# Optimization experiments

Measured on AMD Instinct MI355X. Metric: run time of the kernel, lower is better.

## Reference

```python
import jax, jax.numpy as jnp
import numpy as np

WORLD_SIZE = 1
EXPERT_NUM = 8
D_MODEL = 1024
D_HIDDEN = 4096
TOK_PER_EXPERT = 2048


def setup_inputs() -> dict:
    key = jax.random.key(0)
    k1, k2, k3 = jax.random.split(key, 3)
    x = jax.random.normal(k1, (EXPERT_NUM, TOK_PER_EXPERT, D_MODEL), dtype=jnp.float32)
    # kaiming_uniform-like scale for faithfulness of magnitudes
    bound1 = 1.0 / np.sqrt(D_MODEL)
    bound2 = 1.0 / np.sqrt(D_HIDDEN)
    weight1 = jax.random.uniform(k2, (EXPERT_NUM, D_HIDDEN, D_MODEL), dtype=jnp.float32, minval=-bound1, maxval=bound1)
    weight2 = jax.random.uniform(k3, (EXPERT_NUM, D_MODEL, D_HIDDEN), dtype=jnp.float32, minval=-bound2, maxval=bound2)
    return {"x": x, "weight1": weight1, "weight2": weight2}


def reference(x, weight1, weight2):
    # x -> (world_size, expert_num, tokens, d_model)
    xr = x.reshape(WORLD_SIZE, EXPERT_NUM, -1, D_MODEL)
    # grouped GEMM 1 + ReLU: [g,e,s,m] x [e,h,m] -> [g,e,s,h]
    ffn1 = jax.nn.relu(jnp.einsum('gesm,ehm->gesh', xr, weight1))
    # grouped GEMM 2: [g,e,s,h] x [e,m,h] -> [g,e,s,m]
    y = jnp.einsum('gesh,emh->gesm', ffn1, weight2)
    return y
```

## Files before the change

### kernel.cpp

```cpp
#include <hip/hip_runtime.h>
#include <hip/hip_bf16.h>

#define EXPERTS 8
#define TOK 2048
#define DM 1024
#define DH 4096

#define BM 128
#define BN 128
#define BK 32
#define LSTR 40

typedef __bf16 bf16x8 __attribute__((ext_vector_type(8)));
typedef float  f32x4  __attribute__((ext_vector_type(4)));

static __device__ __forceinline__ bf16x8 cvt8(float4 a, float4 b) {
    bf16x8 r;
    r[0] = (__bf16)a.x; r[1] = (__bf16)a.y; r[2] = (__bf16)a.z; r[3] = (__bf16)a.w;
    r[4] = (__bf16)b.x; r[5] = (__bf16)b.y; r[6] = (__bf16)b.z; r[7] = (__bf16)b.w;
    return r;
}

static __device__ __forceinline__ void gload16(const __bf16* g, __bf16* l) {
    __builtin_amdgcn_global_load_lds(
        (__attribute__((address_space(1))) void*)g,
        (__attribute__((address_space(3))) void*)l, 16, 0, 0);
}

#define BARRIER() asm volatile("s_barrier" ::: "memory")
#define LGKM0()   do { asm volatile("s_waitcnt lgkmcnt(0)" ::: "memory"); \
                       __builtin_amdgcn_sched_barrier(0); } while (0)
#define LGKM8()   asm volatile("s_waitcnt lgkmcnt(8)" ::: "memory")
#define VMW4()    asm volatile("s_waitcnt vmcnt(4)" ::: "memory")
#define VMW0()    asm volatile("s_waitcnt vmcnt(0)" ::: "memory")

__global__ __launch_bounds__(256)
void cvt_all(const float* __restrict__ x,  const float* __restrict__ w1,
             const float* __restrict__ w2, __bf16* __restrict__ xb,
             __bf16* __restrict__ w1b,     __bf16* __restrict__ w2b,
             int nx, int nw1, int ntot) {
    int i = blockIdx.x * blockDim.x + threadIdx.x;
    const int stride = gridDim.x * blockDim.x;
    for (; i < ntot; i += stride) {
        const float* src; __bf16* dst; int off;
        if (i < nx)            { src = x;  dst = xb;  off = i; }
        else if (i < nx + nw1) { src = w1; dst = w1b; off = i - nx; }
        else                   { src = w2; dst = w2b; off = i - nx - nw1; }
        const float4* p = (const float4*)src + (size_t)off * 2;
        float4 a = p[0], b = p[1];
        *((bf16x8*)dst + off) = cvt8(a, b);
    }
}

template<bool RELU, bool OUT_BF16>
__global__ __launch_bounds__(512, 2)
void gemm8(const __bf16* __restrict__ Ap, const __bf16* __restrict__ Bp,
           void* __restrict__ Cp, int N, int K, int tiles_m, int tiles_n,
           size_t sA, size_t sB, size_t sC)
{
    __shared__ __bf16 lds[2][2][16384];

    int bid = blockIdx.x;
    const int chunk = gridDim.x >> 3;
    bid = (bid & 7) * chunk + (bid >> 3);

    const int per_e = tiles_m * tiles_n;
    const int e  = bid / per_e;
    const int tt = bid - e * per_e;
    const int tn = tt / tiles_m;
    const int tm = tt - tn * tiles_m;

    const int tid = threadIdx.x;
    const int l   = tid & 63;
    const int wid = tid >> 6;
    const int wr  = wid >> 2;
    const int wc  = wid & 3;
    const int lr  = l & 15;
    const int kg  = l >> 4;
    const int lq  = l >> 3;
    const int swz_e = ((l & 7) ^ lq) << 3;

    const int cc0  = (kg * 16) ^ ((l & 7) << 4);
    const int cc1  = cc0 ^ 64;
    const int rowA = (wr * 128 + lr) * 128;
    const int rowB = (wc * 64  + lr) * 128;

    const __bf16* Ag = Ap + e * sA + (size_t)(tm * 256) * K;
    const __bf16* Bg = Bp + e * sB + (size_t)(tn * 256) * K;

    auto stage_half = [&](const __bf16* g, int mat, int c2, int h, int kt2) {
        const __bf16* s0 = g + (size_t)(h * 128 + wid * 8 + lq) * K + kt2 * 64 + swz_e;
        gload16(s0,                  &lds[c2][mat][h * 8192 + wid * 512]);
        gload16(s0 + (size_t)64 * K, &lds[c2][mat][h * 8192 + 4096 + wid * 512]);
    };

    f32x4 acc[8][4];
    #pragma unroll
    for (int m = 0; m < 8; ++m)
        #pragma unroll
        for (int n = 0; n < 4; ++n)
            acc[m][n] = (f32x4){0.f, 0.f, 0.f, 0.f};

    const char* A0b = (const char*)&lds[0][0][0] + rowA;
    const char* B0b = (const char*)&lds[0][1][0] + rowB;
    const char* A1b = (const char*)&lds[1][0][0] + rowA;
    const char* B1b = (const char*)&lds[1][1][0] + rowB;

    bf16x8 al[4][2], ah[4][2], bl[2][2], bh[2][2];

    auto rdA = [&](bf16x8 (&dst)[4][2], const char* base, int half) {
        #pragma unroll
        for (int mf = 0; mf < 4; ++mf) {
            dst[mf][0] = *(const bf16x8*)(base + (half * 4 + mf) * 2048 + cc0);
            dst[mf][1] = *(const bf16x8*)(base + (half * 4 + mf) * 2048 + cc1);
        }
    };
    auto rdB = [&](bf16x8 (&dst)[2][2], const char* base, int half) {
        #pragma unroll
        for (int nf = 0; nf < 2; ++nf) {
            dst[nf][0] = *(const bf16x8*)(base + (half * 2 + nf) * 2048 + cc0);
            dst[nf][1] = *(const bf16x8*)(base + (half * 2 + nf) * 2048 + cc1);
        }
    };
    auto mma16 = [&](bf16x8 (&af)[4][2], bf16x8 (&bf_)[2][2], int mo, int no) {
        __builtin_amdgcn_s_setprio(1);
        #pragma unroll
        for (int mf = 0; mf < 4; ++mf)
            #pragma unroll
            for (int nf = 0; nf < 2; ++nf) {
                acc[mo + mf][no + nf] = __builtin_amdgcn_mfma_f32_16x16x32_bf16(af[mf][0], bf_[nf][0], acc[mo + mf][no + nf], 0, 0, 0);
                acc[mo + mf][no + nf] = __builtin_amdgcn_mfma_f32_16x16x32_bf16(af[mf][1], bf_[nf][1], acc[mo + mf][no + nf], 0, 0, 0);
            }
        __builtin_amdgcn_s_setprio(0);
    };

    const int NT = K / 64;
    const int NI = NT / 2;

    stage_half(Ag, 0, 0, 0, 0); stage_half(Ag, 0, 0, 1, 0);
    stage_half(Bg, 1, 0, 0, 0); stage_half(Bg, 1, 0, 1, 0);
    stage_half(Bg, 1, 1, 0, 1); stage_half(Bg, 1, 1, 1, 1);
    VMW4();
    BARRIER();

    for (int it = 0; it < NI; ++it) {
        const int To = 2 * it + 1;
        const int Te = 2 * it + 2;
        const int Tn = 2 * it + 3;
        const bool pf = (it + 1 < NI);

        rdA(al, A0b, 0); rdB(bl, B0b, 0);
        stage_half(Ag, 0, 1, 0, To);
        LGKM8();
        BARRIER(); LGKM0();
        mma16(al, bl, 0, 0);
        BARRIER();

        rdB(bh, B0b, 1);
        stage_half(Ag, 0, 1, 1, To);
        BARRIER(); LGKM0();
        mma16(al, bh, 0, 2);
        BARRIER();

        rdA(ah, A0b, 1);
        if (pf) stage_half(Bg, 1, 0, 0, Te);
        BARRIER(); LGKM0();
        mma16(ah, bh, 4, 2);
        BARRIER();

        if (pf) stage_half(Bg, 1, 0, 1, Te);
        BARRIER();
        mma16(ah, bl, 4, 0);
        if (pf) VMW4(); else VMW0();
        BARRIER();

        rdA(al, A1b, 0); rdB(bl, B1b, 0);
        if (pf) stage_half(Ag, 0, 0, 0, Te);
        LGKM8();
        BARRIER(); LGKM0();
        mma16(al, bl, 0, 0);
        BARRIER();

        rdB(bh, B1b, 1);
        if (pf) stage_half(Ag, 0, 0, 1, Te);
        BARRIER(); LGKM0();
        mma16(al, bh, 0, 2);
        BARRIER();

        rdA(ah, A1b, 1);
        if (pf) stage_half(Bg, 1, 1, 0, Tn);
        BARRIER(); LGKM0();
        mma16(ah, bh, 4, 2);
        BARRIER();

        if (pf) stage_half(Bg, 1, 1, 1, Tn);
        BARRIER();
        mma16(ah, bl, 4, 0);
        if (pf) VMW4();
        BARRIER();
    }

    const int orow = tm * 256 + wr * 128 + kg * 4;
    const int ocol = tn * 256 + wc * 64 + lr;
    if constexpr (OUT_BF16) {
        __bf16* C = (__bf16*)Cp + e * sC;
        #pragma unroll
        for (int mf = 0; mf < 8; ++mf)
            #pragma unroll
            for (int j = 0; j < 4; ++j) {
                const size_t base = (size_t)(orow + mf * 16 + j) * N + ocol;
                #pragma unroll
                for (int nf = 0; nf < 4; ++nf) {
                    float v = acc[mf][nf][j];
                    if (RELU) v = fmaxf(v, 0.f);
                    C[base + nf * 16] = (__bf16)v;
                }
            }
    } else {
        float* C = (float*)Cp + e * sC;
        #pragma unroll
        for (int mf = 0; mf < 8; ++mf)
            #pragma unroll
            for (int j = 0; j < 4; ++j) {
                const size_t base = (size_t)(orow + mf * 16 + j) * N + ocol;
                #pragma unroll
                for (int nf = 0; nf < 4; ++nf) {
                    float v = acc[mf][nf][j];
                    if (RELU) v = fmaxf(v, 0.f);
                    C[base + nf * 16] = v;
                }
            }
    }
}

template<int AMODE, int BMODE, bool RELU, bool OUT_BF16>
__global__ __launch_bounds__(256)
void gemm2(const void* __restrict__ Ap, const void* __restrict__ Bp,
           void* __restrict__ Cp, int N, int K, int tiles_m, int tiles_n,
           size_t sA, size_t sB, size_t sC)
{
    constexpr int LA = (AMODE == 0) ? BK : LSTR;
    constexpr int LB = (BMODE == 0) ? BK : LSTR;
    __shared__ __bf16 As[BM * LA];
    __shared__ __bf16 Bs[BN * LB];

    int bid = blockIdx.x;
    const int chunk = gridDim.x >> 3;
    bid = (bid & 7) * chunk + (bid >> 3);

    const int per_e = tiles_m * tiles_n;
    const int e  = bid / per_e;
    const int t  = bid - e * per_e;
    const int tn = t / tiles_m;
    const int tm = t - tn * tiles_m;

    const int tid = threadIdx.x;
    const int l   = tid & 63;
    const int wid = tid >> 6;
    const int wr  = wid >> 1, wc = wid & 1;
    const int lr  = l & 15;
    const int kg  = l >> 4;
    const int srow = tid >> 1;
    const int scol = (tid & 1) << 4;

    const __bf16* gA = nullptr; __bf16* lA = nullptr;
    const float*  pAf = nullptr; __bf16* aWr = nullptr;
    float4 A0, A1, A2, A3;
    if constexpr (AMODE == 0) {
        gA = (const __bf16*)Ap + e * sA
           + (size_t)(tm * BM + wid * 16 + (l >> 2)) * K + (l & 3) * 8;
        lA = As + wid * 512;
    } else {
        pAf = (const float*)Ap + e * sA + (size_t)(tm * BM + srow) * K + scol;
        aWr = As + srow * LA + scol;
        A0 = *(const float4*)(pAf);      A1 = *(const float4*)(pAf + 4);
        A2 = *(const float4*)(pAf + 8);  A3 = *(const float4*)(pAf + 12);
    }
    const __bf16* gB = nullptr; __bf16* lB = nullptr;
    const float*  pBf = nullptr; __bf16* bWr = nullptr;
    float4 B0, B1, B2, B3;
    if constexpr (BMODE == 0) {
        gB = (const __bf16*)Bp + e * sB
           + (size_t)(tn * BN + wid * 16 + (l >> 2)) * K + (l & 3) * 8;
        lB = Bs + wid * 512;
    } else {
        pBf = (const float*)Bp + e * sB + (size_t)(tn * BN + srow) * K + scol;
        bWr = Bs + srow * LB + scol;
        B0 = *(const float4*)(pBf);      B1 = *(const float4*)(pBf + 4);
        B2 = *(const float4*)(pBf + 8);  B3 = *(const float4*)(pBf + 12);
    }

    const __bf16* aRd = As + (wr * 64 + lr) * LA + kg * 8;
    const __bf16* bRd = Bs + (wc * 64 + lr) * LB + kg * 8;

    f32x4 acc[4][4];
    #pragma unroll
    for (int m = 0; m < 4; ++m)
        #pragma unroll
        for (int n = 0; n < 4; ++n)
            acc[m][n] = (f32x4){0.f, 0.f, 0.f, 0.f};

    const int NT = K / BK;
    for (int kt = 0; kt < NT; ++kt) {
        if (kt) __syncthreads();
        if constexpr (AMODE == 0) {
            gload16(gA, lA);
            gload16(gA + (size_t)64 * K, lA + 2048);
            gA += BK;
        } else {
            *(bf16x8*)(aWr)     = cvt8(A0, A1);
            *(bf16x8*)(aWr + 8) = cvt8(A2, A3);
        }
        if constexpr (BMODE == 0) {
            gload16(gB, lB);
            gload16(gB + (size_t)64 * K, lB + 2048);
            gB += BK;
        } else {
            *(bf16x8*)(bWr)     = cvt8(B0, B1);
            *(bf16x8*)(bWr + 8) = cvt8(B2, B3);
        }
        __syncthreads();

        if (kt + 1 < NT) {
            if constexpr (AMODE == 2) {
                pAf += BK;
                A0 = *(const float4*)(pAf);      A1 = *(const float4*)(pAf + 4);
                A2 = *(const float4*)(pAf + 8);  A3 = *(const float4*)(pAf + 12);
            }
            if constexpr (BMODE == 2) {
                pBf += BK;
                B0 = *(const float4*)(pBf);      B1 = *(const float4*)(pBf + 4);
                B2 = *(const float4*)(pBf + 8);  B3 = *(const float4*)(pBf + 12);
            }
        }

        bf16x8 af[4], bfr[4];
        #pragma unroll
        for (int m = 0; m < 4; ++m) af[m]  = *(const bf16x8*)(aRd + m * 16 * LA);
        #pragma unroll
        for (int n = 0; n < 4; ++n) bfr[n] = *(const bf16x8*)(bRd + n * 16 * LB);
        #pragma unroll
        for (int m = 0; m < 4; ++m)
            #pragma unroll
            for (int n = 0; n < 4; ++n)
                acc[m][n] = __builtin_amdgcn_mfma_f32_16x16x32_bf16(af[m], bfr[n], acc[m][n], 0, 0, 0);
    }

    const int orow = tm * BM + wr * 64 + kg * 4;
    const int ocol = tn * BN + wc * 64 + lr;
    if constexpr (OUT_BF16) {
        __bf16* C = (__bf16*)Cp + e * sC;
        #pragma unroll
        for (int m = 0; m < 4; ++m)
            #pragma unroll
            for (int j = 0; j < 4; ++j) {
                const size_t base = (size_t)(orow + m * 16 + j) * N + ocol;
                #pragma unroll
                for (int n = 0; n < 4; ++n) {
                    float v = acc[m][n][j];
                    if (RELU) v = fmaxf(v, 0.f);
                    C[base + n * 16] = (__bf16)v;
                }
            }
    } else {
        float* C = (float*)Cp + e * sC;
        #pragma unroll
        for (int m = 0; m < 4; ++m)
            #pragma unroll
            for (int j = 0; j < 4; ++j) {
                const size_t base = (size_t)(orow + m * 16 + j) * N + ocol;
                #pragma unroll
                for (int n = 0; n < 4; ++n) {
                    float v = acc[m][n][j];
                    if (RELU) v = fmaxf(v, 0.f);
                    C[base + n * 16] = v;
                }
            }
    }
}

extern "C" void kernel_launch(void* const* d_in, const int* in_sizes, int n_in,
                              void* d_out, int out_size, void* d_ws, size_t ws_size,
                              hipStream_t stream) {
    const float* x  = (const float*)d_in[0];
    const float* w1 = (const float*)d_in[1];
    const float* w2 = (const float*)d_in[2];
    float* out = (float*)d_out;

    const size_t SZ_F  = (size_t)EXPERTS * TOK * DH * sizeof(__bf16);
    const size_t SZ_X  = (size_t)EXPERTS * TOK * DM * sizeof(__bf16);
    const size_t SZ_W1 = (size_t)EXPERTS * DH * DM * sizeof(__bf16);
    const size_t SZ_W2 = (size_t)EXPERTS * DM * DH * sizeof(__bf16);

    char* wsb = (char*)d_ws;
    __bf16* ffn1 = (__bf16*)wsb;

    const dim3 blk(256);
    const dim3 cgrid(2048);
    const int NX  = EXPERTS * TOK * DM / 8;
    const int NW1 = EXPERTS * DH * DM / 8;
    const int NW2 = EXPERTS * DM * DH / 8;

    const size_t eA1 = (size_t)TOK * DM, eB1 = (size_t)DH * DM, eC1 = (size_t)TOK * DH;
    const size_t eA2 = (size_t)TOK * DH, eB2 = (size_t)DM * DH, eC2 = (size_t)TOK * DM;

    if (ws_size >= SZ_F + SZ_X + SZ_W1 + SZ_W2) {
        __bf16* xb  = (__bf16*)(wsb + SZ_F);
        __bf16* w1b = (__bf16*)(wsb + SZ_F + SZ_X);
        __bf16* w2b = (__bf16*)(wsb + SZ_F + SZ_X + SZ_W1);
        hipLaunchKernelGGL(cvt_all, cgrid, blk, 0, stream,
            x, w1, w2, xb, w1b, w2b, NX, NW1, NX + NW1 + NW2);
        const dim3 g1(EXPERTS * (TOK / 256) * (DH / 256));
        const dim3 g2(EXPERTS * (TOK / 256) * (DM / 256));
        hipLaunchKernelGGL((gemm8<true, true>), g1, dim3(512), 0, stream,
            xb, w1b, ffn1, DH, DM, TOK / 256, DH / 256, eA1, eB1, eC1);
        hipLaunchKernelGGL((gemm8<false, false>), g2, dim3(512), 0, stream,
            ffn1, w2b, out, DM, DH, TOK / 256, DM / 256, eA2, eB2, eC2);
    } else if (ws_size >= SZ_F + SZ_X + SZ_W1) {
        __bf16* xb  = (__bf16*)(wsb + SZ_F);
        __bf16* w1b = (__bf16*)(wsb + SZ_F + SZ_X);
        hipLaunchKernelGGL(cvt_all, cgrid, blk, 0, stream,
            x, w1, w1, xb, w1b, w1b, NX, NW1, NX + NW1);
        const dim3 g1(EXPERTS * (TOK / 256) * (DH / 256));
        const dim3 g2(EXPERTS * (TOK / BM) * (DM / BN));
        hipLaunchKernelGGL((gemm8<true, true>), g1, dim3(512), 0, stream,
            xb, w1b, ffn1, DH, DM, TOK / 256, DH / 256, eA1, eB1, eC1);
        hipLaunchKernelGGL((gemm2<0, 2, false, false>), g2, blk, 0, stream,
            ffn1, w2, out, DM, DH, TOK / BM, DM / BN, eA2, eB2, eC2);
    } else if (ws_size >= SZ_F + SZ_W1) {
        __bf16* w1b = (__bf16*)(wsb + SZ_F);
        hipLaunchKernelGGL(cvt_all, cgrid, blk, 0, stream,
            w1, w1, w1, w1b, w1b, w1b, NW1, 0, NW1);
        const dim3 g1(EXPERTS * (TOK / BM) * (DH / BN));
        const dim3 g2(EXPERTS * (TOK / BM) * (DM / BN));
        hipLaunchKernelGGL((gemm2<2, 0, true, true>), g1, blk, 0, stream,
            x, w1b, ffn1, DH, DM, TOK / BM, DH / BN, eA1, eB1, eC1);
        hipLaunchKernelGGL((gemm2<0, 2, false, false>), g2, blk, 0, stream,
            ffn1, w2, out, DM, DH, TOK / BM, DM / BN, eA2, eB2, eC2);
    } else if (ws_size >= SZ_F) {
        const dim3 g1(EXPERTS * (TOK / BM) * (DH / BN));
        const dim3 g2(EXPERTS * (TOK / BM) * (DM / BN));
        hipLaunchKernelGGL((gemm2<2, 2, true, true>), g1, blk, 0, stream,
            x, w1, ffn1, DH, DM, TOK / BM, DH / BN, eA1, eB1, eC1);
        hipLaunchKernelGGL((gemm2<0, 2, false, false>), g2, blk, 0, stream,
            ffn1, w2, out, DM, DH, TOK / BM, DM / BN, eA2, eB2, eC2);
    } else {
        int rows = (int)((ws_size / ((size_t)DH * sizeof(__bf16))) / BM) * BM;
        if (rows <= 0) rows = BM;
        if (rows > TOK) rows = TOK;
        for (int e = 0; e < EXPERTS; ++e) {
            for (int r0 = 0; r0 < TOK; r0 += rows) {
                int mr = (TOK - r0 < rows) ? (TOK - r0) : rows;
                dim3 cg1((mr / BM) * (DH / BN));
                hipLaunchKernelGGL((gemm2<2, 2, true, true>), cg1, blk, 0, stream,
                    x + ((size_t)e * TOK + r0) * DM, w1 + (size_t)e * DH * DM, ffn1,
                    DH, DM, mr / BM, DH / BN, (size_t)0, (size_t)0, (size_t)0);
                dim3 cg2((mr / BM) * (DM / BN));
                hipLaunchKernelGGL((gemm2<0, 2, false, false>), cg2, blk, 0, stream,
                    ffn1, w2 + (size_t)e * DM * DH, out + ((size_t)e * TOK + r0) * DM,
                    DM, DH, mr / BM, DM / BN, (size_t)0, (size_t)0, (size_t)0);
            }
        }
    }
}
```

Baseline: 349.5 us.

## Restructure GEMM main loop into software-pipelined LDS reads with fewer barriers

Rewrites the grouped-GEMM k-loop from an 8-phase, barrier-heavy schedule into a single-tile-per-iteration pipeline. LDS fragment reads for the next phase (and the next tile's low fragments) are interleaved with MFMA blocks, and fine-grained lgkmcnt waits replace full drains. Both A and B stages for tile 1 are now prefetched up front, with one vmcnt wait per tile. The goal is fewer s_barriers and hiding LDS latency behind MFMAs, at the cost of more live registers and trickier hazard correctness on the double buffers.

```diff
diff --git a/kernel.cpp b/kernel.cpp
--- a/kernel.cpp
+++ b/kernel.cpp
@@ -28,11 +28,10 @@
 }
 
 #define BARRIER() asm volatile("s_barrier" ::: "memory")
-#define LGKM0()   do { asm volatile("s_waitcnt lgkmcnt(0)" ::: "memory"); \
-                       __builtin_amdgcn_sched_barrier(0); } while (0)
-#define LGKM8()   asm volatile("s_waitcnt lgkmcnt(8)" ::: "memory")
-#define VMW4()    asm volatile("s_waitcnt vmcnt(4)" ::: "memory")
-#define VMW0()    asm volatile("s_waitcnt vmcnt(0)" ::: "memory")
+#define SB()      __builtin_amdgcn_sched_barrier(0)
+#define LGKM(n)   do { asm volatile("s_waitcnt lgkmcnt(" #n ")" ::: "memory"); SB(); } while (0)
+#define VMW0()    do { asm volatile("s_waitcnt vmcnt(0)" ::: "memory"); SB(); } while (0)
+#define VMW8()    do { asm volatile("s_waitcnt vmcnt(8)" ::: "memory"); SB(); } while (0)
 
 __global__ __launch_bounds__(256)
 void cvt_all(const float* __restrict__ x,  const float* __restrict__ w1,
@@ -101,27 +100,15 @@
         for (int n = 0; n < 4; ++n)
             acc[m][n] = (f32x4){0.f, 0.f, 0.f, 0.f};
 
-    const char* A0b = (const char*)&lds[0][0][0] + rowA;
-    const char* B0b = (const char*)&lds[0][1][0] + rowB;
-    const char* A1b = (const char*)&lds[1][0][0] + rowA;
-    const char* B1b = (const char*)&lds[1][1][0] + rowB;
+    const char* Abs[2] = { (const char*)&lds[0][0][0] + rowA,
+                           (const char*)&lds[1][0][0] + rowA };
+    const char* Bbs[2] = { (const char*)&lds[0][1][0] + rowB,
+                           (const char*)&lds[1][1][0] + rowB };
 
     bf16x8 al[4][2], ah[4][2], bl[2][2], bh[2][2];
 
-    auto rdA = [&](bf16x8 (&dst)[4][2], const char* base, int half) {
-        #pragma unroll
-        for (int mf = 0; mf < 4; ++mf) {
-            dst[mf][0] = *(const bf16x8*)(base + (half * 4 + mf) * 2048 + cc0);
-            dst[mf][1] = *(const bf16x8*)(base + (half * 4 + mf) * 2048 + cc1);
-        }
-    };
-    auto rdB = [&](bf16x8 (&dst)[2][2], const char* base, int half) {
-        #pragma unroll
-        for (int nf = 0; nf < 2; ++nf) {
-            dst[nf][0] = *(const bf16x8*)(base + (half * 2 + nf) * 2048 + cc0);
-            dst[nf][1] = *(const bf16x8*)(base + (half * 2 + nf) * 2048 + cc1);
-        }
-    };
+    #define RD(base, r, cc) (*(const bf16x8*)((base) + (r) * 2048 + (cc)))
+
     auto mma16 = [&](bf16x8 (&af)[4][2], bf16x8 (&bf_)[2][2], int mo, int no) {
         __builtin_amdgcn_s_setprio(1);
         #pragma unroll
@@ -135,70 +122,72 @@
     };
 
     const int NT = K / 64;
-    const int NI = NT / 2;
 
     stage_half(Ag, 0, 0, 0, 0); stage_half(Ag, 0, 0, 1, 0);
     stage_half(Bg, 1, 0, 0, 0); stage_half(Bg, 1, 0, 1, 0);
+    stage_half(Ag, 0, 1, 0, 1); stage_half(Ag, 0, 1, 1, 1);
     stage_half(Bg, 1, 1, 0, 1); stage_half(Bg, 1, 1, 1, 1);
-    VMW4();
+    VMW8();
     BARRIER();
-
-    for (int it = 0; it < NI; ++it) {
-        const int To = 2 * it + 1;
-        const int Te = 2 * it + 2;
-        const int Tn = 2 * it + 3;
-        const bool pf = (it + 1 < NI);
-
-        rdA(al, A0b, 0); rdB(bl, B0b, 0);
-        stage_half(Ag, 0, 1, 0, To);
-        LGKM8();
-        BARRIER(); LGKM0();
+    {
+        const char* Ab = Abs[0]; const char* Bb = Bbs[0];
+        al[0][0] = RD(Ab, 0, cc0); al[1][0] = RD(Ab, 1, cc0);
+        al[2][0] = RD(Ab, 2, cc0); al[3][0] = RD(Ab, 3, cc0);
+        al[0][1] = RD(Ab, 0, cc1); al[1][1] = RD(Ab, 1, cc1);
+        al[2][1] = RD(Ab, 2, cc1); al[3][1] = RD(Ab, 3, cc1);
+        bl[0][0] = RD(Bb, 0, cc0); bl[1][0] = RD(Bb, 1, cc0);
+        bl[0][1] = RD(Bb, 0, cc1); bl[1][1] = RD(Bb, 1, cc1);
+    }
+
+    for (int t = 0; t < NT; ++t) {
+        const int c = t & 1;
+        const char* Ab  = Abs[c];
+        const char* Bb  = Bbs[c];
+        const char* Abn = Abs[c ^ 1];
+        const char* Bbn = Bbs[c ^ 1];
+        const bool pf1 = (t + 1 < NT);
+        const bool pf2 = (t + 2 < NT);
+
+        SB();
+        bh[0][0] = RD(Bb, 2, cc0); bh[1][0] = RD(Bb, 3, cc0);
+        bh[0][1] = RD(Bb, 2, cc1); bh[1][1] = RD(Bb, 3, cc1);
+        ah[0][0] = RD(Ab, 4, cc0); ah[1][0] = RD(Ab, 5, cc0);
+        LGKM(6);
         mma16(al, bl, 0, 0);
+
+        SB();
+        ah[2][0] = RD(Ab, 6, cc0); ah[3][0] = RD(Ab, 7, cc0);
+        ah[0][1] = RD(Ab, 4, cc1); ah[1][1] = RD(Ab, 5, cc1);
+        ah[2][1] = RD(Ab, 6, cc1); ah[3][1] = RD(Ab, 7, cc1);
+        LGKM(8);
+        VMW0();
         BARRIER();
-
-        rdB(bh, B0b, 1);
-        stage_half(Ag, 0, 1, 1, To);
-        BARRIER(); LGKM0();
+        if (pf2) { stage_half(Bg, 1, c, 0, t + 2); stage_half(Bg, 1, c, 1, t + 2); }
         mma16(al, bh, 0, 2);
+
+        SB();
+        if (pf1) {
+            al[0][0] = RD(Abn, 0, cc0); al[1][0] = RD(Abn, 1, cc0);
+            al[2][0] = RD(Abn, 2, cc0); al[3][0] = RD(Abn, 3, cc0);
+            al[0][1] = RD(Abn, 0, cc1); al[1][1] = RD(Abn, 1, cc1);
+            LGKM(6);
+        } else {
+            LGKM(0);
+        }
         BARRIER();
-
-        rdA(ah, A0b, 1);
-        if (pf) stage_half(Bg, 1, 0, 0, Te);
-        BARRIER(); LGKM0();
+        if (pf2) { stage_half(Ag, 0, c, 0, t + 2); stage_half(Ag, 0, c, 1, t + 2); }
         mma16(ah, bh, 4, 2);
-        BARRIER();
-
-        if (pf) stage_half(Bg, 1, 0, 1, Te);
-        BARRIER();
+
+        SB();
         mma16(ah, bl, 4, 0);
-        if (pf) VMW4(); else VMW0();
-        BARRIER();
-
-        rdA(al, A1b, 0); rdB(bl, B1b, 0);
-        if (pf) stage_half(Ag, 0, 0, 0, Te);
-        LGKM8();
-        BARRIER(); LGKM0();
-        mma16(al, bl, 0, 0);
-        BARRIER();
-
-        rdB(bh, B1b, 1);
-        if (pf) stage_half(Ag, 0, 0, 1, Te);
-        BARRIER(); LGKM0();
-        mma16(al, bh, 0, 2);
-        BARRIER();
-
-        rdA(ah, A1b, 1);
-        if (pf) stage_half(Bg, 1, 1, 0, Tn);
-        BARRIER(); LGKM0();
-        mma16(ah, bh, 4, 2);
-        BARRIER();
-
-        if (pf) stage_half(Bg, 1, 1, 1, Tn);
-        BARRIER();
-        mma16(ah, bl, 4, 0);
-        if (pf) VMW4();
-        BARRIER();
-    }
+        SB();
+        if (pf1) {
+            al[2][1] = RD(Abn, 2, cc1); al[3][1] = RD(Abn, 3, cc1);
+            bl[0][0] = RD(Bbn, 0, cc0); bl[1][0] = RD(Bbn, 1, cc0);
+            bl[0][1] = RD(Bbn, 0, cc1); bl[1][1] = RD(Bbn, 1, cc1);
+        }
+    }
+    #undef RD
 
     const int orow = tm * 256 + wr * 128 + kg * 4;
     const int ocol = tn * 256 + wc * 64 + lr;
```

Measured after the change: 466.1 us. 33.4% more time.
